# Kernel optimization log

Measured on AMD Instinct MI355X. Metric: run time of the kernel, lower is better.

Reference implementation:

```python
import jax, jax.numpy as jnp
import numpy as np

N, E, C, H = 50000, 1_600_000, 128, 128
NUM_GRAPHS = 64


def setup_inputs() -> dict:
    key = jax.random.key(0)
    ks = jax.random.split(key, 9)
    x = jax.random.normal(ks[0], (N, C), dtype=jnp.float32)
    edge_index = jax.random.randint(ks[1], (2, E), 0, N, dtype=jnp.int64)
    edge_index_neg = jax.random.randint(ks[2], (2, E), 0, N, dtype=jnp.int64)
    batch = jnp.sort(jax.random.randint(ks[3], (N,), 0, NUM_GRAPHS, dtype=jnp.int64))
    W1 = jax.random.normal(ks[4], (C, H), dtype=jnp.float32) * 0.05
    b1 = jnp.zeros((H,), dtype=jnp.float32)
    W2 = jax.random.normal(ks[5], (H, H), dtype=jnp.float32) * 0.05
    b2 = jnp.zeros((H,), dtype=jnp.float32)
    We = jax.random.normal(ks[6], (2 * H, 1), dtype=jnp.float32) * 0.05
    be = jnp.zeros((1,), dtype=jnp.float32)
    return {"x": x, "edge_index": edge_index, "edge_index_neg": edge_index_neg,
            "batch": batch, "W1": W1, "b1": b1, "W2": W2, "b2": b2,
            "We": We, "be": be}


def reference(x, edge_index, edge_index_neg, batch, W1, b1, W2, b2, We, be):
    # x_enc: Linear -> ReLU -> Linear, then outer ReLU activation (eval mode, dropout=0)
    h = jax.nn.relu(jnp.dot(x, W1) + b1)          # [N, H]
    h = jax.nn.relu(jnp.dot(h, W2) + b2)          # [N, H]
    # p_e_x(cat([q, k])) == q @ We[:H] + k @ We[H:] + be  (avoids materializing cat)
    hdim = W1.shape[1]
    Wq, Wk = We[:hdim], We[hdim:]                  # [H,1] each

    def edge_score(ei):
        q = h[ei[0]]                               # [E, H] gather
        k = h[ei[1]]                               # [E, H] gather
        return jnp.dot(q, Wq) + jnp.dot(k, Wk) + be  # [E, 1]

    e_pred_pos = edge_score(edge_index)
    e_pred_neg = edge_score(edge_index_neg)
    return (e_pred_pos, e_pred_neg, edge_index_neg)
```

## Files before the change

### kernel.cpp

```cpp
#include <hip/hip_runtime.h>

#define CDIM 128
#define HDIM 128
#define LIM  40960

typedef short bf16x8 __attribute__((ext_vector_type(8)));
typedef float f32x16 __attribute__((ext_vector_type(16)));

static __device__ __forceinline__ short f2bf(float f) {
    union { float f; unsigned u; } v; v.f = f;
    unsigned r = v.u + 0x7FFFu + ((v.u >> 16) & 1u);
    return (short)(r >> 16);
}
static __device__ __forceinline__ unsigned pack2(float a, float b) {
    return (unsigned)(unsigned short)f2bf(a) | ((unsigned)(unsigned short)f2bf(b) << 16);
}

__global__ __launch_bounds__(512) void node_mfma(
    const float* __restrict__ x,
    const float* __restrict__ W1, const float* __restrict__ b1,
    const float* __restrict__ W2, const float* __restrict__ b2,
    const float* __restrict__ We,
    unsigned* __restrict__ tab, int N)
{
    __shared__ __align__(16) short wf[16384];
    __shared__ __align__(16) float cv[512];

    const int tid = threadIdx.x;
    const int l   = tid & 63;
    const int col = l & 31;
    const int hi  = l >> 5;
    const int node = blockIdx.x * 256 + (tid >> 6) * 32 + col;

    const int nclamp = (node < N) ? node : (N - 1);
    const float* xb = &x[(size_t)nclamp * CDIM + hi * 8];
    float4 xr[16];
#pragma unroll
    for (int ks = 0; ks < 8; ks++) {
        xr[2 * ks]     = *(const float4*)(xb + ks * 16);
        xr[2 * ks + 1] = *(const float4*)(xb + ks * 16 + 4);
    }

#pragma unroll
    for (int t = 0; t < 4; t++) {
        int rem = t * 512 + tid;
        int lv = rem & 63, ks = (rem >> 6) & 7, ct = rem >> 9;
        int k0 = ks * 16 + 8 * (lv >> 5);
        int n  = ct * 32 + (lv & 31);
        bf16x8 wv;
#pragma unroll
        for (int j = 0; j < 8; j++) wv[j] = f2bf(W1[(k0 + j) * HDIM + n]);
        *(bf16x8*)&wf[rem * 8] = wv;
    }
    if (tid < 512)
        cv[tid] = (tid < 128) ? b1[tid] : (tid < 256) ? b2[tid - 128] : We[tid - 256];

    bf16x8 af[8];
#pragma unroll
    for (int ks = 0; ks < 8; ks++) {
        float4 v0 = xr[2 * ks], v1 = xr[2 * ks + 1];
        af[ks][0] = f2bf(v0.x); af[ks][1] = f2bf(v0.y);
        af[ks][2] = f2bf(v0.z); af[ks][3] = f2bf(v0.w);
        af[ks][4] = f2bf(v1.x); af[ks][5] = f2bf(v1.y);
        af[ks][6] = f2bf(v1.z); af[ks][7] = f2bf(v1.w);
    }
    __syncthreads();

    const f32x16 zz = {0.f,0.f,0.f,0.f,0.f,0.f,0.f,0.f,0.f,0.f,0.f,0.f,0.f,0.f,0.f,0.f};

    f32x16 acc[4];
#pragma unroll
    for (int ct = 0; ct < 4; ct++) acc[ct] = zz;
#pragma unroll
    for (int ks = 0; ks < 8; ks++) {
#pragma unroll
        for (int ct = 0; ct < 4; ct++) {
            bf16x8 wfrag = *(const bf16x8*)&wf[((ct * 8 + ks) * 64 + l) * 8];
            acc[ct] = __builtin_amdgcn_mfma_f32_32x32x16_bf16(wfrag, af[ks], acc[ct], 0, 0, 0);
        }
    }

    unsigned P[4][4][2], Q[4][4][2];
#pragma unroll
    for (int ct = 0; ct < 4; ct++) {
#pragma unroll
        for (int g = 0; g < 4; g++) {
            float4 bv = *(const float4*)&cv[32 * ct + 8 * g + 4 * hi];
            float h0  = fmaxf(acc[ct][4 * g + 0] + bv.x, 0.f);
            float h1v = fmaxf(acc[ct][4 * g + 1] + bv.y, 0.f);
            float h2v = fmaxf(acc[ct][4 * g + 2] + bv.z, 0.f);
            float h3v = fmaxf(acc[ct][4 * g + 3] + bv.w, 0.f);
            P[ct][g][0] = pack2(h0, h1v);
            P[ct][g][1] = pack2(h2v, h3v);
        }
    }
#pragma unroll
    for (int ct = 0; ct < 4; ct++)
#pragma unroll
        for (int g = 0; g < 4; g++)
#pragma unroll
            for (int p = 0; p < 2; p++)
                Q[ct][g][p] = (unsigned)__shfl_xor((int)P[ct][g][p], 32, 64);

    __syncthreads();

#pragma unroll
    for (int t = 0; t < 4; t++) {
        int rem = t * 512 + tid;
        int lv = rem & 63, ks = (rem >> 6) & 7, ct = rem >> 9;
        int k0 = ks * 16 + 8 * (lv >> 5);
        int n  = ct * 32 + (lv & 31);
        bf16x8 wv;
#pragma unroll
        for (int j = 0; j < 8; j++) wv[j] = f2bf(W2[(k0 + j) * HDIM + n]);
        *(bf16x8*)&wf[rem * 8] = wv;
    }
    __syncthreads();

    f32x16 acc2[4];
#pragma unroll
    for (int ct = 0; ct < 4; ct++) acc2[ct] = zz;
#pragma unroll
    for (int ks2 = 0; ks2 < 8; ks2++) {
        const int c  = ks2 >> 1;
        const int s2 = (ks2 & 1) * 2;
        union { bf16x8 v; unsigned u[4]; } bb;
        bb.u[0] = hi ? Q[c][s2 + 1][0] : P[c][s2][0];
        bb.u[1] = hi ? Q[c][s2 + 1][1] : P[c][s2][1];
        bb.u[2] = hi ? P[c][s2 + 1][0] : Q[c][s2][0];
        bb.u[3] = hi ? P[c][s2 + 1][1] : Q[c][s2][1];
#pragma unroll
        for (int ct = 0; ct < 4; ct++) {
            bf16x8 wfrag = *(const bf16x8*)&wf[((ct * 8 + ks2) * 64 + l) * 8];
            acc2[ct] = __builtin_amdgcn_mfma_f32_32x32x16_bf16(wfrag, bb.v, acc2[ct], 0, 0, 0);
        }
    }

    float pq = 0.f, pk = 0.f;
#pragma unroll
    for (int ct = 0; ct < 4; ct++) {
#pragma unroll
        for (int g = 0; g < 4; g++) {
            float4 b2v = *(const float4*)&cv[128 + 32 * ct + 8 * g + 4 * hi];
            float4 wqv = *(const float4*)&cv[256 + 32 * ct + 8 * g + 4 * hi];
            float4 wkv = *(const float4*)&cv[384 + 32 * ct + 8 * g + 4 * hi];
            const float* b2a = (const float*)&b2v;
            const float* wqa = (const float*)&wqv;
            const float* wka = (const float*)&wkv;
#pragma unroll
            for (int i = 0; i < 4; i++) {
                float hv = fmaxf(acc2[ct][4 * g + i] + b2a[i], 0.f);
                pq = fmaf(hv, wqa[i], pq);
                pk = fmaf(hv, wka[i], pk);
            }
        }
    }
    pq += __shfl_xor(pq, 32, 64);
    pk += __shfl_xor(pk, 32, 64);
    if (hi == 0 && node < N) tab[node] = pack2(pq, pk);
}

__global__ __launch_bounds__(1024) void edge_kernel(
    const int* __restrict__ eip, const int* __restrict__ ein,
    const unsigned* __restrict__ tab, const float* __restrict__ be_p,
    float* __restrict__ out, int E)
{
    __shared__ __align__(16) unsigned lt[LIM];
    const int tid = threadIdx.x;
    const int wv = tid >> 6, ln = tid & 63;

    const int U = E >> 2;
    const int chunk = (U + gridDim.x - 1) / gridDim.x;
    const int ustart = blockIdx.x * chunk;
    const int uend = min(U, ustart + chunk);

    const int4* eip4 = (const int4*)eip;
    const int4* ein4 = (const int4*)ein;
    float4* out4 = (float4*)out;

    const int u0 = ustart + tid, u1 = u0 + 1024;
    const bool v0 = u0 < uend, v1 = u1 < uend;

    int4 ns0 = {0,0,0,0}, nd0 = {0,0,0,0}, ns1 = {0,0,0,0}, nd1 = {0,0,0,0};
    int4 ps0 = {0,0,0,0}, pd0 = {0,0,0,0};
    if (v0) { ns0 = ein4[u0]; nd0 = ein4[U + u0]; ps0 = eip4[u0]; pd0 = eip4[U + u0]; }
    if (v1) { ns1 = ein4[u1]; nd1 = ein4[U + u1]; }
    __builtin_amdgcn_sched_barrier(0);

    const uint4* tg4 = (const uint4*)tab;
#pragma unroll
    for (int t = 0; t < LIM / 4 / 1024; t++) {
        int c = (t * 16 + wv) * 64;
        __builtin_amdgcn_global_load_lds(
            (const __attribute__((address_space(1))) void*)(tg4 + c + ln),
            (__attribute__((address_space(3))) void*)((char*)lt + (size_t)c * 16),
            16, 0, 0);
    }
    __builtin_amdgcn_sched_barrier(0);

    if (v0) {
        out4[2 * U + u0] = make_float4((float)ns0.x, (float)ns0.y, (float)ns0.z, (float)ns0.w);
        out4[3 * U + u0] = make_float4((float)nd0.x, (float)nd0.y, (float)nd0.z, (float)nd0.w);
    }
    if (v1) {
        out4[2 * U + u1] = make_float4((float)ns1.x, (float)ns1.y, (float)ns1.z, (float)ns1.w);
        out4[3 * U + u1] = make_float4((float)nd1.x, (float)nd1.y, (float)nd1.z, (float)nd1.w);
    }
    __syncthreads();

    const float be = be_p[0];
#define GATHER(i) ((i) < LIM ? lt[i] : tab[i])
#define SCORE(us, ud) (__uint_as_float((us) << 16) + __uint_as_float((ud) & 0xFFFF0000u) + be)

    int4 ps1 = {0,0,0,0}, pd1 = {0,0,0,0};
    if (v1) { ps1 = eip4[u1]; pd1 = eip4[U + u1]; }

    if (v0) {
        unsigned a0 = GATHER(ps0.x), a1 = GATHER(ps0.y), a2 = GATHER(ps0.z), a3 = GATHER(ps0.w);
        unsigned b0 = GATHER(pd0.x), b1 = GATHER(pd0.y), b2 = GATHER(pd0.z), b3 = GATHER(pd0.w);
        out4[u0] = make_float4(SCORE(a0,b0), SCORE(a1,b1), SCORE(a2,b2), SCORE(a3,b3));
        unsigned c0 = GATHER(ns0.x), c1 = GATHER(ns0.y), c2 = GATHER(ns0.z), c3 = GATHER(ns0.w);
        unsigned d0 = GATHER(nd0.x), d1 = GATHER(nd0.y), d2 = GATHER(nd0.z), d3 = GATHER(nd0.w);
        out4[U + u0] = make_float4(SCORE(c0,d0), SCORE(c1,d1), SCORE(c2,d2), SCORE(c3,d3));
    }
    if (v1) {
        unsigned a0 = GATHER(ps1.x), a1 = GATHER(ps1.y), a2 = GATHER(ps1.z), a3 = GATHER(ps1.w);
        unsigned b0 = GATHER(pd1.x), b1 = GATHER(pd1.y), b2 = GATHER(pd1.z), b3 = GATHER(pd1.w);
        out4[u1] = make_float4(SCORE(a0,b0), SCORE(a1,b1), SCORE(a2,b2), SCORE(a3,b3));
        unsigned c0 = GATHER(ns1.x), c1 = GATHER(ns1.y), c2 = GATHER(ns1.z), c3 = GATHER(ns1.w);
        unsigned d0 = GATHER(nd1.x), d1 = GATHER(nd1.y), d2 = GATHER(nd1.z), d3 = GATHER(nd1.w);
        out4[U + u1] = make_float4(SCORE(c0,d0), SCORE(c1,d1), SCORE(c2,d2), SCORE(c3,d3));
    }
#undef GATHER
#undef SCORE
}

extern "C" void kernel_launch(void* const* d_in, const int* in_sizes, int n_in,
                              void* d_out, int out_size, void* d_ws, size_t ws_size,
                              hipStream_t stream) {
    const float* x   = (const float*)d_in[0];
    const int*   eip = (const int*)d_in[1];
    const int*   ein = (const int*)d_in[2];
    const float* W1  = (const float*)d_in[4];
    const float* b1  = (const float*)d_in[5];
    const float* W2  = (const float*)d_in[6];
    const float* b2  = (const float*)d_in[7];
    const float* We  = (const float*)d_in[8];
    const float* be  = (const float*)d_in[9];

    const int N = in_sizes[0] / CDIM;
    const int E = in_sizes[1] / 2;

    unsigned* tab = (unsigned*)d_ws;

    node_mfma<<<(N + 255) / 256, 512, 0, stream>>>(x, W1, b1, W2, b2, We, tab, N);
    edge_kernel<<<256, 1024, 0, stream>>>(eip, ein, tab, be, (float*)d_out, E);
}
```

Measured before the change: 28.55 us.

## Move part of negative-edge index copy into idle blocks of node kernel

The node MLP kernel now launches a fixed grid of 256 blocks. The blocks beyond those needed for nodes copy the first 40% of the negative edge_index (int to float) into the output. The edge kernel skips that prefix, which shortens its store-heavy phase and overlaps the copy with the MFMA node computation. The risk is that the extra blocks compete for bandwidth with the node kernel, and that the fixed 256-block grid assumes N fits in fewer blocks. Nodes would go uncomputed if N > 65536.

```diff
diff --git a/kernel.cpp b/kernel.cpp
--- a/kernel.cpp
+++ b/kernel.cpp
@@ -20,17 +20,35 @@
     const float* __restrict__ x,
     const float* __restrict__ W1, const float* __restrict__ b1,
     const float* __restrict__ W2, const float* __restrict__ b2,
-    const float* __restrict__ We,
-    unsigned* __restrict__ tab, int N)
+    const float* __restrict__ We, const int* __restrict__ ein,
+    unsigned* __restrict__ tab, float* __restrict__ out,
+    int N, int E, int CS)
 {
     __shared__ __align__(16) short wf[16384];
     __shared__ __align__(16) float cv[512];
 
     const int tid = threadIdx.x;
+    const int blk = blockIdx.x;
+    const int NB  = (N + 255) >> 8;
+    const int U   = E >> 2;
+
+    if (blk >= NB) {
+        const int NC = (int)gridDim.x - NB;
+        const int4* ein4 = (const int4*)ein;
+        float4* o4 = (float4*)out;
+        for (int i = (blk - NB) * 512 + tid; i < CS; i += NC * 512) {
+            int4 v = ein4[i];
+            o4[2 * U + i] = make_float4((float)v.x, (float)v.y, (float)v.z, (float)v.w);
+            int4 w = ein4[U + i];
+            o4[3 * U + i] = make_float4((float)w.x, (float)w.y, (float)w.z, (float)w.w);
+        }
+        return;
+    }
+
     const int l   = tid & 63;
     const int col = l & 31;
     const int hi  = l >> 5;
-    const int node = blockIdx.x * 256 + (tid >> 6) * 32 + col;
+    const int node = blk * 256 + (tid >> 6) * 32 + col;
 
     const int nclamp = (node < N) ? node : (N - 1);
     const float* xb = &x[(size_t)nclamp * CDIM + hi * 8];
@@ -52,8 +70,7 @@
         for (int j = 0; j < 8; j++) wv[j] = f2bf(W1[(k0 + j) * HDIM + n]);
         *(bf16x8*)&wf[rem * 8] = wv;
     }
-    if (tid < 512)
-        cv[tid] = (tid < 128) ? b1[tid] : (tid < 256) ? b2[tid - 128] : We[tid - 256];
+    cv[tid] = (tid < 128) ? b1[tid] : (tid < 256) ? b2[tid - 128] : We[tid - 256];
 
     bf16x8 af[8];
 #pragma unroll
@@ -163,7 +180,7 @@
 __global__ __launch_bounds__(1024) void edge_kernel(
     const int* __restrict__ eip, const int* __restrict__ ein,
     const unsigned* __restrict__ tab, const float* __restrict__ be_p,
-    float* __restrict__ out, int E)
+    float* __restrict__ out, int E, int CS)
 {
     __shared__ __align__(16) unsigned lt[LIM];
     const int tid = threadIdx.x;
@@ -198,11 +215,11 @@
     }
     __builtin_amdgcn_sched_barrier(0);
 
-    if (v0) {
+    if (v0 && u0 >= CS) {
         out4[2 * U + u0] = make_float4((float)ns0.x, (float)ns0.y, (float)ns0.z, (float)ns0.w);
         out4[3 * U + u0] = make_float4((float)nd0.x, (float)nd0.y, (float)nd0.z, (float)nd0.w);
     }
-    if (v1) {
+    if (v1 && u1 >= CS) {
         out4[2 * U + u1] = make_float4((float)ns1.x, (float)ns1.y, (float)ns1.z, (float)ns1.w);
         out4[3 * U + u1] = make_float4((float)nd1.x, (float)nd1.y, (float)nd1.z, (float)nd1.w);
     }
@@ -250,9 +267,12 @@
 
     const int N = in_sizes[0] / CDIM;
     const int E = in_sizes[1] / 2;
+    const int U = E >> 2;
+    const int CS = (U * 2) / 5;
 
     unsigned* tab = (unsigned*)d_ws;
 
-    node_mfma<<<(N + 255) / 256, 512, 0, stream>>>(x, W1, b1, W2, b2, We, tab, N);
-    edge_kernel<<<256, 1024, 0, stream>>>(eip, ein, tab, be, (float*)d_out, E);
-}
+    node_mfma<<<256, 512, 0, stream>>>(x, W1, b1, W2, b2, We, ein, tab,
+                                       (float*)d_out, N, E, CS);
+    edge_kernel<<<256, 1024, 0, stream>>>(eip, ein, tab, be, (float*)d_out, E, CS);
+}
```

After: 29.39 us. +2.9%, slower.
